# Kernel tuning notes

Measured on AMD Instinct MI355X. Metric: run time of the kernel, lower is better.

Reference implementation:

```python
import jax, jax.numpy as jnp
import numpy as np

B, L, D = 4, 4096, 256


def setup_inputs() -> dict:
    key = jax.random.key(0)
    k_x, k_q, k_k, k_v, k_w, k_b = jax.random.split(key, 6)
    s = 1.0 / np.sqrt(D)
    return {
        "x": jax.random.normal(k_x, (B, L, D), dtype=jnp.float32),
        "Wq": jax.random.normal(k_q, (D, D), dtype=jnp.float32) * s,   # nn.Linear weight (out,in)
        "Wk": jax.random.normal(k_k, (D, D), dtype=jnp.float32) * s,
        "Wv": jax.random.normal(k_v, (D, D), dtype=jnp.float32) * s,
        "w_mlp": jax.random.normal(k_w, (D,), dtype=jnp.float32) * s,  # Linear(D,1) weight
        "b_mlp": jnp.zeros((), dtype=jnp.float32),                     # Linear(D,1) bias
    }


def reference(x, Wq, Wk, Wv, w_mlp, b_mlp):
    # Projections (nn.Linear: y = x @ W.T, no bias)
    Q = jnp.einsum("bld,ed->ble", x, Wq)
    K = jnp.einsum("bld,ed->ble", x, Wk)
    V = jnp.einsum("bld,ed->ble", x, Wv)
    # score[b,i,j] = relu((Q[b,i]-K[b,j]) @ w_mlp + b_mlp)
    # decomposed: (Q-K)@w = Q@w - K@w  (exact same math, no (B,L,L,D) tensor)
    q_s = Q @ w_mlp  # (B,L)
    k_s = K @ w_mlp  # (B,L)
    scores = jax.nn.relu(q_s[:, :, None] - k_s[:, None, :] + b_mlp)  # (B,L,L)
    attn = jax.nn.softmax(scores, axis=-1)  # softmax over key axis j
    # out[b,i,d] = sum_j attn[b,i,j] * V[b,j,d]
    out = jnp.einsum("bij,bjd->bid", attn, V)
    return out  # dropout p=0.0 is identity
```

## Files before the change

### kernel.cpp

```cpp
#include <hip/hip_runtime.h>
#include <math.h>

#define BB 4
#define LL 4096
#define DD 256
#define NROWS (BB*LL)
#define CHUNK 32
#define NC (LL/CHUNK)
#define NB 8192

typedef __bf16 bf16x8 __attribute__((ext_vector_type(8)));
typedef __bf16 bf16x4 __attribute__((ext_vector_type(4)));
typedef float floatx4 __attribute__((ext_vector_type(4)));

__global__ void k_prep(const float* __restrict__ Wq, const float* __restrict__ Wk,
                       const float* __restrict__ Wv, const float* __restrict__ w,
                       float* __restrict__ u_part,
                       __bf16* __restrict__ Wh, __bf16* __restrict__ Wl) {
    __shared__ float wl[16];
    int d = threadIdx.x;
    int e0 = blockIdx.x * 16;
    if (d < 16) wl[d] = w[e0 + d];
    __syncthreads();
    float aq = 0.f, ak = 0.f;
    #pragma unroll
    for (int j = 0; j < 16; ++j) {
        float we = wl[j];
        aq = fmaf(Wq[(size_t)(e0 + j)*DD + d], we, aq);
        ak = fmaf(Wk[(size_t)(e0 + j)*DD + d], we, ak);
        float wv = Wv[(size_t)(e0 + j)*DD + d];
        __bf16 h = (__bf16)wv;
        Wh[(size_t)(e0 + j)*DD + d] = h;
        Wl[(size_t)(e0 + j)*DD + d] = (__bf16)(wv - (float)h);
    }
    u_part[(size_t)blockIdx.x*512 + d]       = aq;
    u_part[(size_t)blockIdx.x*512 + DD + d]  = ak;
}

__global__ void __launch_bounds__(256) k_gemm_mfma(
        const float* __restrict__ x,
        const __bf16* __restrict__ Wh, const __bf16* __restrict__ Wl,
        const float* __restrict__ u_part, const float* __restrict__ bmlp,
        float* __restrict__ V, float* __restrict__ a, float* __restrict__ c) {
    __shared__ __bf16 Ah[2][32*40];
    __shared__ __bf16 Al[2][32*40];
    __shared__ float4 ul[128];
    __shared__ float pros[512];
    const int tid = threadIdx.x;
    const int wave = tid >> 6, lane = tid & 63;
    const int rowBase = blockIdx.x * 32;
    const int colBase = blockIdx.y * 128;
    const int quad = lane >> 4, l16 = lane & 15;
    const int srow = tid >> 3, skq = (tid & 7) * 4;
    const bool doproj = (blockIdx.y == 0);

    if (doproj && tid < 128) {
        float4 s = make_float4(0.f, 0.f, 0.f, 0.f);
        #pragma unroll
        for (int g = 0; g < 16; ++g) {
            float4 p = *(const float4*)(u_part + (size_t)g*512 + tid*4);
            s.x += p.x; s.y += p.y; s.z += p.z; s.w += p.w;
        }
        ul[tid] = s;
    }
    __syncthreads();

    floatx4 acc[2][2];
    #pragma unroll
    for (int rt = 0; rt < 2; ++rt)
        #pragma unroll
        for (int ct = 0; ct < 2; ++ct)
            acc[rt][ct] = (floatx4){0.f, 0.f, 0.f, 0.f};
    float aq = 0.f, ak = 0.f;

    const float* xrow = x + (size_t)(rowBase + srow)*DD + skq;

    {
        float4 xv = *(const float4*)xrow;
        __bf16 h0 = (__bf16)xv.x, h1 = (__bf16)xv.y, h2 = (__bf16)xv.z, h3 = (__bf16)xv.w;
        bf16x4 hv = {h0, h1, h2, h3};
        bf16x4 lv = {(__bf16)(xv.x - (float)h0), (__bf16)(xv.y - (float)h1),
                     (__bf16)(xv.z - (float)h2), (__bf16)(xv.w - (float)h3)};
        *(bf16x4*)&Ah[0][srow*40 + skq] = hv;
        *(bf16x4*)&Al[0][srow*40 + skq] = lv;
        if (doproj) {
            float4 q4 = ul[(tid & 7)];
            float4 k4 = ul[64 + (tid & 7)];
            aq = fmaf(xv.x, q4.x, fmaf(xv.y, q4.y, fmaf(xv.z, q4.z, fmaf(xv.w, q4.w, aq))));
            ak = fmaf(xv.x, k4.x, fmaf(xv.y, k4.y, fmaf(xv.z, k4.z, fmaf(xv.w, k4.w, ak))));
        }
    }
    __syncthreads();

    for (int t = 0; t < 8; ++t) {
        const int k0 = t * 32;
        const int cur = t & 1;
        float4 xv;
        if (t < 7) xv = *(const float4*)(xrow + k0 + 32);
        bf16x8 ah[2], al[2];
        #pragma unroll
        for (int rt = 0; rt < 2; ++rt) {
            int m = rt*16 + l16;
            ah[rt] = *(bf16x8*)&Ah[cur][m*40 + quad*8];
            al[rt] = *(bf16x8*)&Al[cur][m*40 + quad*8];
        }
        if (t < 7) {
            __bf16 h0 = (__bf16)xv.x, h1 = (__bf16)xv.y, h2 = (__bf16)xv.z, h3 = (__bf16)xv.w;
            bf16x4 hv = {h0, h1, h2, h3};
            bf16x4 lv = {(__bf16)(xv.x - (float)h0), (__bf16)(xv.y - (float)h1),
                         (__bf16)(xv.z - (float)h2), (__bf16)(xv.w - (float)h3)};
            *(bf16x4*)&Ah[cur^1][srow*40 + skq] = hv;
            *(bf16x4*)&Al[cur^1][srow*40 + skq] = lv;
            if (doproj) {
                float4 q4 = ul[((k0 + 32) >> 2) + (tid & 7)];
                float4 k4 = ul[64 + ((k0 + 32) >> 2) + (tid & 7)];
                aq = fmaf(xv.x, q4.x, fmaf(xv.y, q4.y, fmaf(xv.z, q4.z, fmaf(xv.w, q4.w, aq))));
                ak = fmaf(xv.x, k4.x, fmaf(xv.y, k4.y, fmaf(xv.z, k4.z, fmaf(xv.w, k4.w, ak))));
            }
        }
        __syncthreads();
        #pragma unroll
        for (int ct = 0; ct < 2; ++ct) {
            int n = colBase + wave*32 + ct*16 + l16;
            bf16x8 bh = *(const bf16x8*)(Wh + (size_t)n*DD + k0 + quad*8);
            bf16x8 bl = *(const bf16x8*)(Wl + (size_t)n*DD + k0 + quad*8);
            #pragma unroll
            for (int rt = 0; rt < 2; ++rt) {
                acc[rt][ct] = __builtin_amdgcn_mfma_f32_16x16x32_bf16(ah[rt], bh, acc[rt][ct], 0, 0, 0);
                acc[rt][ct] = __builtin_amdgcn_mfma_f32_16x16x32_bf16(ah[rt], bl, acc[rt][ct], 0, 0, 0);
                acc[rt][ct] = __builtin_amdgcn_mfma_f32_16x16x32_bf16(al[rt], bh, acc[rt][ct], 0, 0, 0);
            }
        }
    }
    #pragma unroll
    for (int rt = 0; rt < 2; ++rt)
        #pragma unroll
        for (int ct = 0; ct < 2; ++ct)
            #pragma unroll
            for (int i = 0; i < 4; ++i) {
                int row = rowBase + rt*16 + quad*4 + i;
                int col = colBase + wave*32 + ct*16 + l16;
                V[(size_t)row*DD + col] = acc[rt][ct][i];
            }
    if (doproj) {
        __syncthreads();
        pros[tid] = aq;
        pros[256 + tid] = ak;
        __syncthreads();
        if (tid < 32) {
            float sa = 0.f, sc = 0.f;
            #pragma unroll
            for (int j = 0; j < 8; ++j) {
                sa += pros[tid*8 + j];
                sc += pros[256 + tid*8 + j];
            }
            a[rowBase + tid] = sa + bmlp[0];
            c[rowBase + tid] = sc;
        }
    }
}

__global__ void __launch_bounds__(1024) k_sortish(const float* __restrict__ c,
        int* __restrict__ binstart_g, int* __restrict__ perm,
        float* __restrict__ c_sorted, float* __restrict__ e_sorted,
        float* __restrict__ SE, float* __restrict__ hdr) {
    __shared__ int   hist[NB];
    __shared__ float esl[LL];
    __shared__ float scrf[64];
    int b = blockIdx.x, tid = threadIdx.x;
    int wave = tid >> 6, lane = tid & 63;
    int* scri = (int*)scrf;

    float4 cv = ((const float4*)(c + (size_t)b*LL))[tid];
    float cw[4] = {cv.x, cv.y, cv.z, cv.w};
    float mn = fminf(fminf(cw[0],cw[1]), fminf(cw[2],cw[3]));
    float mx = fmaxf(fmaxf(cw[0],cw[1]), fmaxf(cw[2],cw[3]));
    #pragma unroll
    for (int off = 32; off > 0; off >>= 1) {
        mn = fminf(mn, __shfl_down(mn, off));
        mx = fmaxf(mx, __shfl_down(mx, off));
    }
    if (lane == 0) { scrf[wave] = mn; scrf[32 + wave] = mx; }
    __syncthreads();
    if (wave == 0) {
        float m = (lane < 16) ? scrf[lane]      :  3.4e38f;
        float M = (lane < 16) ? scrf[32 + lane] : -3.4e38f;
        #pragma unroll
        for (int off = 32; off > 0; off >>= 1) {
            m = fminf(m, __shfl_down(m, off));
            M = fmaxf(M, __shfl_down(M, off));
        }
        if (lane == 0) { scrf[0] = m; scrf[1] = M; }
    }
    __syncthreads();
    float cmin = scrf[0], cmax = scrf[1];
    float scale = (float)NB / fmaxf(cmax - cmin, 1e-20f);
    __syncthreads();

    ((int4*)hist)[tid] = make_int4(0,0,0,0);
    ((int4*)hist)[tid + 1024] = make_int4(0,0,0,0);
    __syncthreads();

    int bins[4];
    #pragma unroll
    for (int u = 0; u < 4; ++u) {
        int bi = (int)((cw[u] - cmin) * scale);
        bi = bi < 0 ? 0 : (bi > NB-1 ? NB-1 : bi);
        bins[u] = bi;
        atomicAdd(&hist[bi], 1);
    }
    __syncthreads();

    int loc[8]; int base = 0;
    #pragma unroll
    for (int j = 0; j < 8; ++j) { loc[j] = base; base += hist[tid*8 + j]; }
    int incl = base;
    #pragma unroll
    for (int off = 1; off < 64; off <<= 1) {
        int t = __shfl_up(incl, off);
        if (lane >= off) incl += t;
    }
    if (lane == 63) scri[wave] = incl;
    __syncthreads();
    if (wave == 0) {
        int v = (lane < 16) ? scri[lane] : 0;
        int s = v;
        #pragma unroll
        for (int off = 1; off < 16; off <<= 1) {
            int t = __shfl_up(s, off);
            if (lane >= off) s += t;
        }
        if (lane < 16) scri[lane] = s - v;
    }
    __syncthreads();
    int thread_excl = (incl - base) + scri[wave];
    __syncthreads();
    #pragma unroll
    for (int j = 0; j < 8; ++j) {
        int bs = thread_excl + loc[j];
        binstart_g[(size_t)b*(NB+2) + tid*8 + j] = bs;
        hist[tid*8 + j] = bs;
    }
    if (tid == 0) {
        binstart_g[(size_t)b*(NB+2) + NB]     = LL;
        binstart_g[(size_t)b*(NB+2) + NB + 1] = LL;
        hdr[b*2 + 0] = cmin;
        hdr[b*2 + 1] = scale;
    }
    __syncthreads();

    #pragma unroll
    for (int u = 0; u < 4; ++u) {
        int i = tid*4 + u;
        int r = atomicAdd(&hist[bins[u]], 1);
        float e = expf(cmin - cw[u]);
        perm[(size_t)b*LL + r] = i;
        c_sorted[(size_t)b*LL + r] = cw[u];
        e_sorted[(size_t)b*LL + r] = e;
        esl[r] = e;
    }
    __syncthreads();

    float le[4]; float s0 = 0.f;
    #pragma unroll
    for (int u = 0; u < 4; ++u) { le[u] = s0; s0 += esl[tid*4 + u]; }
    float fincl = s0;
    #pragma unroll
    for (int off = 1; off < 64; off <<= 1) {
        float t = __shfl_up(fincl, off);
        if (lane >= off) fincl += t;
    }
    if (lane == 63) scrf[wave] = fincl;
    __syncthreads();
    if (wave == 0) {
        float v = (lane < 16) ? scrf[lane] : 0.f;
        float s = v;
        #pragma unroll
        for (int off = 1; off < 16; off <<= 1) {
            float t = __shfl_up(s, off);
            if (lane >= off) s += t;
        }
        if (lane < 16) scrf[lane] = s - v;
    }
    __syncthreads();
    float texcl = (fincl - s0) + scrf[wave];
    #pragma unroll
    for (int u = 0; u < 4; ++u)
        SE[(size_t)b*(LL+1) + tid*4 + u] = texcl + le[u];
    if (tid == 1023) SE[(size_t)b*(LL+1) + LL] = texcl + s0;
}

__global__ void k_scan(const float* __restrict__ V, const int* __restrict__ perm,
        const float* __restrict__ e_sorted,
        float* __restrict__ Pl, float* __restrict__ Pel,
        float* __restrict__ Tp, float* __restrict__ Te) {
    int b = blockIdx.y, q = blockIdx.x;
    int d = threadIdx.x;
    __shared__ int pj[CHUNK];
    __shared__ float pe[CHUNK];
    if (d < CHUNK) {
        pj[d] = perm[(size_t)b*LL + q*CHUNK + d];
        pe[d] = e_sorted[(size_t)b*LL + q*CHUNK + d];
    }
    __syncthreads();
    float vr[CHUNK];
    #pragma unroll
    for (int r = 0; r < CHUNK; ++r)
        vr[r] = V[((size_t)b*LL + pj[r]) * DD + d];
    float acc = 0.f, acce = 0.f;
    size_t kb = (size_t)b*LL + (size_t)q*CHUNK;
    #pragma unroll
    for (int r = 0; r < CHUNK; ++r) {
        size_t o = (kb + r) * DD + d;
        Pl[o]  = acc;
        Pel[o] = acce;
        acc += vr[r];
        acce = fmaf(pe[r], vr[r], acce);
    }
    size_t to = ((size_t)b*NC + q) * DD + d;
    Tp[to] = acc;
    Te[to] = acce;
}

__global__ void k_base(const float* __restrict__ Tp, const float* __restrict__ Te,
        float* __restrict__ baseP, float* __restrict__ basePe) {
    int q = blockIdx.x, b = blockIdx.y, d = threadIdx.x;
    float acc = 0.f, acce = 0.f;
    #pragma unroll 8
    for (int i = 0; i < q; ++i) {
        size_t ti = ((size_t)b*NC + i) * DD + d;
        acc += Tp[ti]; acce += Te[ti];
    }
    size_t o = ((size_t)b*(NC+1) + q) * DD + d;
    baseP[o] = acc; basePe[o] = acce;
}

__global__ void k_out(const float* __restrict__ a, const float* __restrict__ hdr,
                      const int* __restrict__ binstart,
                      const float* __restrict__ c_sorted, const float* __restrict__ e_sorted,
                      const int* __restrict__ perm, const float* __restrict__ V,
                      const float* __restrict__ SE,
                      const float* __restrict__ Pl, const float* __restrict__ Pel,
                      const float* __restrict__ baseP, const float* __restrict__ basePe,
                      float* __restrict__ out) {
    int row = blockIdx.x * 4 + (threadIdx.x >> 6);
    int lane = threadIdx.x & 63;
    int b = row >> 12;
    float ai = a[row];
    float cmin = hdr[b*2 + 0], scale = hdr[b*2 + 1];
    float t = (ai - cmin) * scale;
    int ib = t < 0.f ? 0 : (t >= (float)NB ? NB : (int)t);
    int k    = binstart[(size_t)b*(NB+2) + ib];
    int kend = binstart[(size_t)b*(NB+2) + ib + 1];
    float alpha = expf(cmin - ai);
    float Z = fmaf(alpha, (float)(LL - k), SE[(size_t)b*(LL+1) + k]);
    size_t db = (size_t)lane * 4;
    size_t totoff = ((size_t)b * (NC+1) + NC) * DD + db;
    float4 ptot  = *(const float4*)(baseP  + totoff);
    float4 pk, pek;
    if (k < LL) {
        int q = k >> 5;
        size_t po = ((size_t)b * LL + k) * DD + db;
        size_t bo = ((size_t)b * (NC+1) + q) * DD + db;
        float4 pl = *(const float4*)(Pl    + po);
        float4 bp = *(const float4*)(baseP + bo);
        float4 pe = *(const float4*)(Pel    + po);
        float4 be = *(const float4*)(basePe + bo);
        pk.x = pl.x + bp.x; pk.y = pl.y + bp.y; pk.z = pl.z + bp.z; pk.w = pl.w + bp.w;
        pek.x = pe.x + be.x; pek.y = pe.y + be.y; pek.z = pe.z + be.z; pek.w = pe.w + be.w;
    } else {
        pk = ptot;
        pek = *(const float4*)(basePe + totoff);
    }
    float4 num;
    num.x = fmaf(alpha, ptot.x - pk.x, pek.x);
    num.y = fmaf(alpha, ptot.y - pk.y, pek.y);
    num.z = fmaf(alpha, ptot.z - pk.z, pek.z);
    num.w = fmaf(alpha, ptot.w - pk.w, pek.w);
    for (int r = k; r < kend; ++r) {
        float cr = c_sorted[(size_t)b*LL + r];
        if (cr < ai) {
            float w = e_sorted[(size_t)b*LL + r] - alpha;
            int j = perm[(size_t)b*LL + r];
            float4 v = *(const float4*)(V + ((size_t)b*LL + j) * DD + db);
            num.x = fmaf(w, v.x, num.x);
            num.y = fmaf(w, v.y, num.y);
            num.z = fmaf(w, v.z, num.z);
            num.w = fmaf(w, v.w, num.w);
            Z += w;
        }
    }
    float invZ = 1.f / Z;
    float4 o;
    o.x = num.x * invZ; o.y = num.y * invZ; o.z = num.z * invZ; o.w = num.w * invZ;
    *(float4*)(out + (size_t)row * DD + db) = o;
}

extern "C" void kernel_launch(void* const* d_in, const int* in_sizes, int n_in,
                              void* d_out, int out_size, void* d_ws, size_t ws_size,
                              hipStream_t stream) {
    const float* x  = (const float*)d_in[0];
    const float* Wq = (const float*)d_in[1];
    const float* Wk = (const float*)d_in[2];
    const float* Wv = (const float*)d_in[3];
    const float* wm = (const float*)d_in[4];
    const float* bm = (const float*)d_in[5];
    float* out = (float*)d_out;
    float* ws = (float*)d_ws;

    size_t off = 0;
    auto alloc = [&](size_t n) {
        float* p = ws + off;
        off += (n + 255) & ~(size_t)255;
        return p;
    };
    float* u_part   = alloc(16*512);
    float* a        = alloc(NROWS);
    float* c        = alloc(NROWS);
    float* c_sorted = alloc(NROWS);
    float* e_sorted = alloc(NROWS);
    float* SE       = alloc((size_t)BB*(LL+1));
    int*   perm     = (int*)alloc(NROWS);
    int*   binstart = (int*)alloc((size_t)BB*(NB+2));
    float* hdr      = alloc(2*BB);
    float* V        = alloc((size_t)NROWS*DD);
    float* Pl       = alloc((size_t)NROWS*DD);
    float* Pel      = alloc((size_t)NROWS*DD);
    float* Tp       = alloc((size_t)BB*NC*DD);
    float* Te       = alloc((size_t)BB*NC*DD);
    float* baseP    = alloc((size_t)BB*(NC+1)*DD);
    float* basePe   = alloc((size_t)BB*(NC+1)*DD);
    __bf16* Wh      = (__bf16*)alloc((size_t)DD*DD/2);
    __bf16* Wl      = (__bf16*)alloc((size_t)DD*DD/2);

    hipLaunchKernelGGL(k_prep, dim3(16), dim3(DD), 0, stream, Wq, Wk, Wv, wm, u_part, Wh, Wl);
    hipLaunchKernelGGL(k_gemm_mfma, dim3(NROWS/32, 2), dim3(256), 0, stream,
                       x, Wh, Wl, u_part, bm, V, a, c);
    hipLaunchKernelGGL(k_sortish, dim3(BB), dim3(1024), 0, stream,
                       c, binstart, perm, c_sorted, e_sorted, SE, hdr);
    hipLaunchKernelGGL(k_scan, dim3(NC, BB), dim3(DD), 0, stream, V, perm, e_sorted, Pl, Pel, Tp, Te);
    hipLaunchKernelGGL(k_base, dim3(NC+1, BB), dim3(DD), 0, stream, Tp, Te, baseP, basePe);
    hipLaunchKernelGGL(k_out, dim3(NROWS/4), dim3(256), 0, stream,
                       a, hdr, binstart, c_sorted, e_sorted, perm, V,
                       SE, Pl, Pel, baseP, basePe, out);
}
```

Measured before the change: 135.1 us.

## Fuse chunk scan, base prefix and output into cooperative kernel with LDS prefixes

```diff
diff --git a/kernel.cpp b/kernel.cpp
--- a/kernel.cpp
+++ b/kernel.cpp
@@ -1,5 +1,8 @@
 #include <hip/hip_runtime.h>
+#include <hip/hip_cooperative_groups.h>
 #include <math.h>
+
+namespace cg = cooperative_groups;
 
 #define BB 4
 #define LL 4096
@@ -161,12 +164,16 @@
 }
 
 __global__ void __launch_bounds__(1024) k_sortish(const float* __restrict__ c,
-        int* __restrict__ binstart_g, int* __restrict__ perm,
+        const float* __restrict__ a,
+        int* __restrict__ perm,
         float* __restrict__ c_sorted, float* __restrict__ e_sorted,
-        float* __restrict__ SE, float* __restrict__ hdr) {
+        float* __restrict__ SE, float* __restrict__ hdr,
+        float4* __restrict__ rowrec, int* __restrict__ rbs_g) {
     __shared__ int   hist[NB];
     __shared__ float esl[LL];
     __shared__ float scrf[64];
+    __shared__ int   qhist[132];
+    __shared__ int   rbs[132];
     int b = blockIdx.x, tid = threadIdx.x;
     int wave = tid >> 6, lane = tid & 63;
     int* scri = (int*)scrf;
@@ -199,6 +206,7 @@
 
     ((int4*)hist)[tid] = make_int4(0,0,0,0);
     ((int4*)hist)[tid + 1024] = make_int4(0,0,0,0);
+    if (tid < 132) qhist[tid] = 0;
     __syncthreads();
 
     int bins[4];
@@ -238,14 +246,27 @@
     #pragma unroll
     for (int j = 0; j < 8; ++j) {
         int bs = thread_excl + loc[j];
-        binstart_g[(size_t)b*(NB+2) + tid*8 + j] = bs;
         hist[tid*8 + j] = bs;
     }
     if (tid == 0) {
-        binstart_g[(size_t)b*(NB+2) + NB]     = LL;
-        binstart_g[(size_t)b*(NB+2) + NB + 1] = LL;
         hdr[b*2 + 0] = cmin;
         hdr[b*2 + 1] = scale;
+    }
+    __syncthreads();
+
+    float4 av = ((const float4*)(a + (size_t)b*LL))[tid];
+    float aw[4] = {av.x, av.y, av.z, av.w};
+    int qq[4]; float4 rec[4];
+    #pragma unroll
+    for (int u = 0; u < 4; ++u) {
+        float t = (aw[u] - cmin) * scale;
+        int ibb = t < 0.f ? 0 : (t >= (float)NB ? NB : (int)t);
+        int k   = (ibb == NB)     ? LL : hist[ibb];
+        int ke  = (ibb >= NB - 1) ? LL : hist[ibb + 1];
+        qq[u] = k >> 5;
+        rec[u] = make_float4(aw[u], __int_as_float(k), __int_as_float(ke),
+                             __int_as_float(tid*4 + u));
+        atomicAdd(&qhist[qq[u]], 1);
     }
     __syncthreads();
 
@@ -261,6 +282,29 @@
     }
     __syncthreads();
 
+    if (wave == 0) {
+        int v0 = qhist[2*lane], v1 = qhist[2*lane+1];
+        int ps = v0 + v1;
+        int qi = ps;
+        #pragma unroll
+        for (int off = 1; off < 64; off <<= 1) {
+            int tu = __shfl_up(qi, off);
+            if (lane >= off) qi += tu;
+        }
+        rbs[2*lane]     = qi - ps;
+        rbs[2*lane + 1] = qi - v1;
+        if (lane == 63) { rbs[128] = qi; rbs[129] = qi + qhist[128]; }
+    }
+    __syncthreads();
+    if (tid < 129) qhist[tid] = rbs[tid];
+    if (tid < 130) rbs_g[b*130 + tid] = rbs[tid];
+    __syncthreads();
+    #pragma unroll
+    for (int u = 0; u < 4; ++u) {
+        int r = atomicAdd(&qhist[qq[u]], 1);
+        rowrec[(size_t)b*LL + r] = rec[u];
+    }
+
     float le[4]; float s0 = 0.f;
     #pragma unroll
     for (int u = 0; u < 4; ++u) { le[u] = s0; s0 += esl[tid*4 + u]; }
@@ -290,36 +334,147 @@
     if (tid == 1023) SE[(size_t)b*(LL+1) + LL] = texcl + s0;
 }
 
-__global__ void k_scan(const float* __restrict__ V, const int* __restrict__ perm,
-        const float* __restrict__ e_sorted,
-        float* __restrict__ Pl, float* __restrict__ Pel,
-        float* __restrict__ Tp, float* __restrict__ Te) {
-    int b = blockIdx.y, q = blockIdx.x;
-    int d = threadIdx.x;
-    __shared__ int pj[CHUNK];
-    __shared__ float pe[CHUNK];
-    if (d < CHUNK) {
-        pj[d] = perm[(size_t)b*LL + q*CHUNK + d];
-        pe[d] = e_sorted[(size_t)b*LL + q*CHUNK + d];
+__device__ __forceinline__ void chunk_out_phase(
+    int b, int q, int tid, const float (&vr)[CHUNK], const float* ev_l,
+    float* Plds, float* Pelds,
+    float* bp_l, float* be_l, float* pt_l, float* pe_l,
+    const float* __restrict__ baseP, const float* __restrict__ basePe,
+    const float4* __restrict__ rowrec, const int* __restrict__ rbs_g,
+    const float* __restrict__ SE, const float* __restrict__ hdr,
+    const float* __restrict__ c_sorted, const float* __restrict__ e_sorted,
+    const int* __restrict__ perm, const float* __restrict__ V,
+    float* __restrict__ out)
+{
+    {
+        size_t o  = ((size_t)b*(NC+1) + q)*DD + tid;
+        size_t ot = ((size_t)b*(NC+1) + NC)*DD + tid;
+        bp_l[tid] = baseP[o];  be_l[tid] = basePe[o];
+        pt_l[tid] = baseP[ot]; pe_l[tid] = basePe[ot];
+    }
+    float accp = 0.f, acce = 0.f;
+    #pragma unroll
+    for (int r = 0; r < CHUNK; ++r) {
+        Plds[r*DD + tid] = accp; Pelds[r*DD + tid] = acce;
+        accp += vr[r]; acce = fmaf(ev_l[r], vr[r], acce);
+    }
+    Plds[CHUNK*DD + tid] = accp; Pelds[CHUNK*DD + tid] = acce;
+    __syncthreads();
+    const int wave = tid >> 6, lane = tid & 63;
+    const int db = lane * 4;
+    const float cmin = hdr[b*2];
+    const float4 bp4 = *(const float4*)&bp_l[db];
+    const float4 be4 = *(const float4*)&be_l[db];
+    const float4 pt4 = *(const float4*)&pt_l[db];
+    const int rs = rbs_g[b*130 + q];
+    const int re = rbs_g[b*130 + q + ((q == NC-1) ? 2 : 1)];
+    for (int t = rs + wave; t < re; t += 4) {
+        float4 rr = rowrec[(size_t)b*LL + t];
+        float ai = rr.x;
+        int k    = __float_as_int(rr.y);
+        int kend = __float_as_int(rr.z);
+        int i    = __float_as_int(rr.w);
+        float alpha = expf(cmin - ai);
+        int local = k - q*CHUNK;
+        const float4 pl4 = *(const float4*)&Plds[local*DD + db];
+        const float4 pe4 = *(const float4*)&Pelds[local*DD + db];
+        float Z = fmaf(alpha, (float)(LL - k), SE[(size_t)b*(LL+1) + k]);
+        float4 num;
+        num.x = fmaf(alpha, pt4.x - (pl4.x + bp4.x), pe4.x + be4.x);
+        num.y = fmaf(alpha, pt4.y - (pl4.y + bp4.y), pe4.y + be4.y);
+        num.z = fmaf(alpha, pt4.z - (pl4.z + bp4.z), pe4.z + be4.z);
+        num.w = fmaf(alpha, pt4.w - (pl4.w + bp4.w), pe4.w + be4.w);
+        for (int r = k; r < kend; ++r) {
+            float cr = c_sorted[(size_t)b*LL + r];
+            if (cr < ai) {
+                float w = e_sorted[(size_t)b*LL + r] - alpha;
+                int j = perm[(size_t)b*LL + r];
+                float4 v = *(const float4*)(V + ((size_t)b*LL + j)*DD + db);
+                num.x = fmaf(w, v.x, num.x);
+                num.y = fmaf(w, v.y, num.y);
+                num.z = fmaf(w, v.z, num.z);
+                num.w = fmaf(w, v.w, num.w);
+                Z += w;
+            }
+        }
+        float invZ = 1.f / Z;
+        float4 o;
+        o.x = num.x * invZ; o.y = num.y * invZ; o.z = num.z * invZ; o.w = num.w * invZ;
+        *(float4*)(out + ((size_t)b*LL + i)*DD + db) = o;
+    }
+}
+
+__global__ void __launch_bounds__(256, 2) k_fused(
+    const float* __restrict__ V, const int* __restrict__ perm,
+    const float* __restrict__ e_sorted, const float* __restrict__ c_sorted,
+    const float4* __restrict__ rowrec, const int* __restrict__ rbs_g,
+    const float* __restrict__ SE, const float* __restrict__ hdr,
+    float* __restrict__ Tp, float* __restrict__ Te,
+    float* __restrict__ baseP, float* __restrict__ basePe,
+    float* __restrict__ out)
+{
+    __shared__ float Plds[(CHUNK+1)*DD];
+    __shared__ float Pelds[(CHUNK+1)*DD];
+    __shared__ float bp_l[DD], be_l[DD], pt_l[DD], pe_l[DD];
+    __shared__ float ev_l[CHUNK];
+    __shared__ int   pj_l[CHUNK];
+    const int q = blockIdx.x, b = blockIdx.y, tid = threadIdx.x;
+    if (tid < CHUNK) {
+        pj_l[tid] = perm[(size_t)b*LL + q*CHUNK + tid];
+        ev_l[tid] = e_sorted[(size_t)b*LL + q*CHUNK + tid];
     }
     __syncthreads();
     float vr[CHUNK];
     #pragma unroll
     for (int r = 0; r < CHUNK; ++r)
-        vr[r] = V[((size_t)b*LL + pj[r]) * DD + d];
-    float acc = 0.f, acce = 0.f;
-    size_t kb = (size_t)b*LL + (size_t)q*CHUNK;
+        vr[r] = V[((size_t)b*LL + pj_l[r])*DD + tid];
+    float sp = 0.f, se = 0.f;
+    #pragma unroll
+    for (int r = 0; r < CHUNK; ++r) { sp += vr[r]; se = fmaf(ev_l[r], vr[r], se); }
+    Tp[((size_t)b*NC + q)*DD + tid] = sp;
+    Te[((size_t)b*NC + q)*DD + tid] = se;
+    __threadfence();
+    cg::grid_group grid = cg::this_grid();
+    grid.sync();
+    if (q == 0) {
+        float ap = 0.f, ae = 0.f;
+        #pragma unroll 8
+        for (int i = 0; i < NC; ++i) {
+            size_t o  = ((size_t)b*(NC+1) + i)*DD + tid;
+            size_t ti = ((size_t)b*NC + i)*DD + tid;
+            baseP[o] = ap; basePe[o] = ae;
+            ap += Tp[ti]; ae += Te[ti];
+        }
+        baseP[((size_t)b*(NC+1) + NC)*DD + tid]  = ap;
+        basePe[((size_t)b*(NC+1) + NC)*DD + tid] = ae;
+    }
+    __threadfence();
+    grid.sync();
+    chunk_out_phase(b, q, tid, vr, ev_l, Plds, Pelds, bp_l, be_l, pt_l, pe_l,
+                    baseP, basePe, rowrec, rbs_g, SE, hdr,
+                    c_sorted, e_sorted, perm, V, out);
+}
+
+__global__ void __launch_bounds__(256) k_tot(
+    const float* __restrict__ V, const int* __restrict__ perm,
+    const float* __restrict__ e_sorted,
+    float* __restrict__ Tp, float* __restrict__ Te)
+{
+    __shared__ float ev_l[CHUNK];
+    __shared__ int   pj_l[CHUNK];
+    const int q = blockIdx.x, b = blockIdx.y, tid = threadIdx.x;
+    if (tid < CHUNK) {
+        pj_l[tid] = perm[(size_t)b*LL + q*CHUNK + tid];
+        ev_l[tid] = e_sorted[(size_t)b*LL + q*CHUNK + tid];
+    }
+    __syncthreads();
+    float sp = 0.f, se = 0.f;
     #pragma unroll
     for (int r = 0; r < CHUNK; ++r) {
-        size_t o = (kb + r) * DD + d;
-        Pl[o]  = acc;
-        Pel[o] = acce;
-        acc += vr[r];
-        acce = fmaf(pe[r], vr[r], acce);
-    }
-    size_t to = ((size_t)b*NC + q) * DD + d;
-    Tp[to] = acc;
-    Te[to] = acce;
+        float v = V[((size_t)b*LL + pj_l[r])*DD + tid];
+        sp += v; se = fmaf(ev_l[r], v, se);
+    }
+    Tp[((size_t)b*NC + q)*DD + tid] = sp;
+    Te[((size_t)b*NC + q)*DD + tid] = se;
 }
 
 __global__ void k_base(const float* __restrict__ Tp, const float* __restrict__ Te,
@@ -335,65 +490,32 @@
     baseP[o] = acc; basePe[o] = acce;
 }
 
-__global__ void k_out(const float* __restrict__ a, const float* __restrict__ hdr,
-                      const int* __restrict__ binstart,
-                      const float* __restrict__ c_sorted, const float* __restrict__ e_sorted,
-                      const int* __restrict__ perm, const float* __restrict__ V,
-                      const float* __restrict__ SE,
-                      const float* __restrict__ Pl, const float* __restrict__ Pel,
-                      const float* __restrict__ baseP, const float* __restrict__ basePe,
-                      float* __restrict__ out) {
-    int row = blockIdx.x * 4 + (threadIdx.x >> 6);
-    int lane = threadIdx.x & 63;
-    int b = row >> 12;
-    float ai = a[row];
-    float cmin = hdr[b*2 + 0], scale = hdr[b*2 + 1];
-    float t = (ai - cmin) * scale;
-    int ib = t < 0.f ? 0 : (t >= (float)NB ? NB : (int)t);
-    int k    = binstart[(size_t)b*(NB+2) + ib];
-    int kend = binstart[(size_t)b*(NB+2) + ib + 1];
-    float alpha = expf(cmin - ai);
-    float Z = fmaf(alpha, (float)(LL - k), SE[(size_t)b*(LL+1) + k]);
-    size_t db = (size_t)lane * 4;
-    size_t totoff = ((size_t)b * (NC+1) + NC) * DD + db;
-    float4 ptot  = *(const float4*)(baseP  + totoff);
-    float4 pk, pek;
-    if (k < LL) {
-        int q = k >> 5;
-        size_t po = ((size_t)b * LL + k) * DD + db;
-        size_t bo = ((size_t)b * (NC+1) + q) * DD + db;
-        float4 pl = *(const float4*)(Pl    + po);
-        float4 bp = *(const float4*)(baseP + bo);
-        float4 pe = *(const float4*)(Pel    + po);
-        float4 be = *(const float4*)(basePe + bo);
-        pk.x = pl.x + bp.x; pk.y = pl.y + bp.y; pk.z = pl.z + bp.z; pk.w = pl.w + bp.w;
-        pek.x = pe.x + be.x; pek.y = pe.y + be.y; pek.z = pe.z + be.z; pek.w = pe.w + be.w;
-    } else {
-        pk = ptot;
-        pek = *(const float4*)(basePe + totoff);
-    }
-    float4 num;
-    num.x = fmaf(alpha, ptot.x - pk.x, pek.x);
-    num.y = fmaf(alpha, ptot.y - pk.y, pek.y);
-    num.z = fmaf(alpha, ptot.z - pk.z, pek.z);
-    num.w = fmaf(alpha, ptot.w - pk.w, pek.w);
-    for (int r = k; r < kend; ++r) {
-        float cr = c_sorted[(size_t)b*LL + r];
-        if (cr < ai) {
-            float w = e_sorted[(size_t)b*LL + r] - alpha;
-            int j = perm[(size_t)b*LL + r];
-            float4 v = *(const float4*)(V + ((size_t)b*LL + j) * DD + db);
-            num.x = fmaf(w, v.x, num.x);
-            num.y = fmaf(w, v.y, num.y);
-            num.z = fmaf(w, v.z, num.z);
-            num.w = fmaf(w, v.w, num.w);
-            Z += w;
-        }
-    }
-    float invZ = 1.f / Z;
-    float4 o;
-    o.x = num.x * invZ; o.y = num.y * invZ; o.z = num.z * invZ; o.w = num.w * invZ;
-    *(float4*)(out + (size_t)row * DD + db) = o;
+__global__ void __launch_bounds__(256, 2) k_outf(
+    const float* __restrict__ V, const int* __restrict__ perm,
+    const float* __restrict__ e_sorted, const float* __restrict__ c_sorted,
+    const float4* __restrict__ rowrec, const int* __restrict__ rbs_g,
+    const float* __restrict__ SE, const float* __restrict__ hdr,
+    const float* __restrict__ baseP, const float* __restrict__ basePe,
+    float* __restrict__ out)
+{
+    __shared__ float Plds[(CHUNK+1)*DD];
+    __shared__ float Pelds[(CHUNK+1)*DD];
+    __shared__ float bp_l[DD], be_l[DD], pt_l[DD], pe_l[DD];
+    __shared__ float ev_l[CHUNK];
+    __shared__ int   pj_l[CHUNK];
+    const int q = blockIdx.x, b = blockIdx.y, tid = threadIdx.x;
+    if (tid < CHUNK) {
+        pj_l[tid] = perm[(size_t)b*LL + q*CHUNK + tid];
+        ev_l[tid] = e_sorted[(size_t)b*LL + q*CHUNK + tid];
+    }
+    __syncthreads();
+    float vr[CHUNK];
+    #pragma unroll
+    for (int r = 0; r < CHUNK; ++r)
+        vr[r] = V[((size_t)b*LL + pj_l[r])*DD + tid];
+    chunk_out_phase(b, q, tid, vr, ev_l, Plds, Pelds, bp_l, be_l, pt_l, pe_l,
+                    baseP, basePe, rowrec, rbs_g, SE, hdr,
+                    c_sorted, e_sorted, perm, V, out);
 }
 
 extern "C" void kernel_launch(void* const* d_in, const int* in_sizes, int n_in,
@@ -421,15 +543,14 @@
     float* e_sorted = alloc(NROWS);
     float* SE       = alloc((size_t)BB*(LL+1));
     int*   perm     = (int*)alloc(NROWS);
-    int*   binstart = (int*)alloc((size_t)BB*(NB+2));
     float* hdr      = alloc(2*BB);
     float* V        = alloc((size_t)NROWS*DD);
-    float* Pl       = alloc((size_t)NROWS*DD);
-    float* Pel      = alloc((size_t)NROWS*DD);
     float* Tp       = alloc((size_t)BB*NC*DD);
     float* Te       = alloc((size_t)BB*NC*DD);
     float* baseP    = alloc((size_t)BB*(NC+1)*DD);
     float* basePe   = alloc((size_t)BB*(NC+1)*DD);
+    float4* rowrec  = (float4*)alloc((size_t)NROWS*4);
+    int*   rbs_g    = (int*)alloc(BB*130);
     __bf16* Wh      = (__bf16*)alloc((size_t)DD*DD/2);
     __bf16* Wl      = (__bf16*)alloc((size_t)DD*DD/2);
 
@@ -437,10 +558,33 @@
     hipLaunchKernelGGL(k_gemm_mfma, dim3(NROWS/32, 2), dim3(256), 0, stream,
                        x, Wh, Wl, u_part, bm, V, a, c);
     hipLaunchKernelGGL(k_sortish, dim3(BB), dim3(1024), 0, stream,
-                       c, binstart, perm, c_sorted, e_sorted, SE, hdr);
-    hipLaunchKernelGGL(k_scan, dim3(NC, BB), dim3(DD), 0, stream, V, perm, e_sorted, Pl, Pel, Tp, Te);
-    hipLaunchKernelGGL(k_base, dim3(NC+1, BB), dim3(DD), 0, stream, Tp, Te, baseP, basePe);
-    hipLaunchKernelGGL(k_out, dim3(NROWS/4), dim3(256), 0, stream,
-                       a, hdr, binstart, c_sorted, e_sorted, perm, V,
-                       SE, Pl, Pel, baseP, basePe, out);
-}
+                       c, a, perm, c_sorted, e_sorted, SE, hdr, rowrec, rbs_g);
+
+    {
+        const float*  Vc    = V;
+        const int*    permc = perm;
+        const float*  ec    = e_sorted;
+        const float*  cc    = c_sorted;
+        const float4* rrc   = rowrec;
+        const int*    rbc   = rbs_g;
+        const float*  SEc   = SE;
+        const float*  hc    = hdr;
+        float* Tpp = Tp; float* Tee = Te; float* bP = baseP; float* bPe = basePe;
+        float* op = out;
+        void* kargs[] = { (void*)&Vc, (void*)&permc, (void*)&ec, (void*)&cc,
+                          (void*)&rrc, (void*)&rbc, (void*)&SEc, (void*)&hc,
+                          (void*)&Tpp, (void*)&Tee, (void*)&bP, (void*)&bPe,
+                          (void*)&op };
+        hipError_t cerr = hipLaunchCooperativeKernel((const void*)k_fused,
+                              dim3(NC, BB), dim3(DD), kargs, 0, stream);
+        if (cerr != hipSuccess) {
+            hipLaunchKernelGGL(k_tot, dim3(NC, BB), dim3(DD), 0, stream,
+                               V, perm, e_sorted, Tp, Te);
+            hipLaunchKernelGGL(k_base, dim3(NC+1, BB), dim3(DD), 0, stream,
+                               Tp, Te, baseP, basePe);
+            hipLaunchKernelGGL(k_outf, dim3(NC, BB), dim3(DD), 0, stream,
+                               V, perm, e_sorted, c_sorted, rowrec, rbs_g,
+                               SE, hdr, baseP, basePe, out);
+        }
+    }
+}
```

Result: slower. 316.5 us (+134.2%).

## Drop per-row prefix arrays; recompute in-chunk partial sums in output kernel

Applied to the files above, without the earlier changes.

```diff
diff --git a/kernel.cpp b/kernel.cpp
--- a/kernel.cpp
+++ b/kernel.cpp
@@ -5,21 +5,31 @@
 #define LL 4096
 #define DD 256
 #define NROWS (BB*LL)
-#define CHUNK 32
+#define CHUNK 16
 #define NC (LL/CHUNK)
-#define NB 8192
+#define NB 4096
 
 typedef __bf16 bf16x8 __attribute__((ext_vector_type(8)));
 typedef __bf16 bf16x4 __attribute__((ext_vector_type(4)));
 typedef float floatx4 __attribute__((ext_vector_type(4)));
 
+__device__ __forceinline__ unsigned encf(float f) {
+    unsigned u = __float_as_uint(f);
+    return (u & 0x80000000u) ? ~u : (u | 0x80000000u);
+}
+__device__ __forceinline__ float decf(unsigned u) {
+    return __uint_as_float((u & 0x80000000u) ? (u ^ 0x80000000u) : ~u);
+}
+
 __global__ void k_prep(const float* __restrict__ Wq, const float* __restrict__ Wk,
                        const float* __restrict__ Wv, const float* __restrict__ w,
                        float* __restrict__ u_part,
-                       __bf16* __restrict__ Wh, __bf16* __restrict__ Wl) {
+                       __bf16* __restrict__ Wh, __bf16* __restrict__ Wl,
+                       unsigned* __restrict__ hdru) {
     __shared__ float wl[16];
     int d = threadIdx.x;
     int e0 = blockIdx.x * 16;
+    if (blockIdx.x == 0 && d < 8) hdru[d] = (d & 1) ? 0u : 0xFFFFFFFFu;
     if (d < 16) wl[d] = w[e0 + d];
     __syncthreads();
     float aq = 0.f, ak = 0.f;
@@ -41,7 +51,8 @@
         const float* __restrict__ x,
         const __bf16* __restrict__ Wh, const __bf16* __restrict__ Wl,
         const float* __restrict__ u_part, const float* __restrict__ bmlp,
-        float* __restrict__ V, float* __restrict__ a, float* __restrict__ c) {
+        float* __restrict__ V, float* __restrict__ a, float* __restrict__ c,
+        unsigned* __restrict__ hdru) {
     __shared__ __bf16 Ah[2][32*40];
     __shared__ __bf16 Al[2][32*40];
     __shared__ float4 ul[128];
@@ -156,14 +167,26 @@
             }
             a[rowBase + tid] = sa + bmlp[0];
             c[rowBase + tid] = sc;
+            float mn = sc, mx = sc;
+            #pragma unroll
+            for (int off = 16; off > 0; off >>= 1) {
+                mn = fminf(mn, __shfl_down(mn, off));
+                mx = fmaxf(mx, __shfl_down(mx, off));
+            }
+            if (tid == 0) {
+                int bb = rowBase >> 12;
+                atomicMin(&hdru[bb*2 + 0], encf(mn));
+                atomicMax(&hdru[bb*2 + 1], encf(mx));
+            }
         }
     }
 }
 
 __global__ void __launch_bounds__(1024) k_sortish(const float* __restrict__ c,
+        const unsigned* __restrict__ hdru,
         int* __restrict__ binstart_g, int* __restrict__ perm,
         float* __restrict__ c_sorted, float* __restrict__ e_sorted,
-        float* __restrict__ SE, float* __restrict__ hdr) {
+        float* __restrict__ SE, float* __restrict__ hdrf) {
     __shared__ int   hist[NB];
     __shared__ float esl[LL];
     __shared__ float scrf[64];
@@ -173,32 +196,11 @@
 
     float4 cv = ((const float4*)(c + (size_t)b*LL))[tid];
     float cw[4] = {cv.x, cv.y, cv.z, cv.w};
-    float mn = fminf(fminf(cw[0],cw[1]), fminf(cw[2],cw[3]));
-    float mx = fmaxf(fmaxf(cw[0],cw[1]), fmaxf(cw[2],cw[3]));
-    #pragma unroll
-    for (int off = 32; off > 0; off >>= 1) {
-        mn = fminf(mn, __shfl_down(mn, off));
-        mx = fmaxf(mx, __shfl_down(mx, off));
-    }
-    if (lane == 0) { scrf[wave] = mn; scrf[32 + wave] = mx; }
-    __syncthreads();
-    if (wave == 0) {
-        float m = (lane < 16) ? scrf[lane]      :  3.4e38f;
-        float M = (lane < 16) ? scrf[32 + lane] : -3.4e38f;
-        #pragma unroll
-        for (int off = 32; off > 0; off >>= 1) {
-            m = fminf(m, __shfl_down(m, off));
-            M = fmaxf(M, __shfl_down(M, off));
-        }
-        if (lane == 0) { scrf[0] = m; scrf[1] = M; }
-    }
-    __syncthreads();
-    float cmin = scrf[0], cmax = scrf[1];
+    float cmin = decf(hdru[b*2 + 0]);
+    float cmax = decf(hdru[b*2 + 1]);
     float scale = (float)NB / fmaxf(cmax - cmin, 1e-20f);
-    __syncthreads();
 
     ((int4*)hist)[tid] = make_int4(0,0,0,0);
-    ((int4*)hist)[tid + 1024] = make_int4(0,0,0,0);
     __syncthreads();
 
     int bins[4];
@@ -211,9 +213,9 @@
     }
     __syncthreads();
 
-    int loc[8]; int base = 0;
-    #pragma unroll
-    for (int j = 0; j < 8; ++j) { loc[j] = base; base += hist[tid*8 + j]; }
+    int loc[4]; int base = 0;
+    #pragma unroll
+    for (int j = 0; j < 4; ++j) { loc[j] = base; base += hist[tid*4 + j]; }
     int incl = base;
     #pragma unroll
     for (int off = 1; off < 64; off <<= 1) {
@@ -236,16 +238,16 @@
     int thread_excl = (incl - base) + scri[wave];
     __syncthreads();
     #pragma unroll
-    for (int j = 0; j < 8; ++j) {
+    for (int j = 0; j < 4; ++j) {
         int bs = thread_excl + loc[j];
-        binstart_g[(size_t)b*(NB+2) + tid*8 + j] = bs;
-        hist[tid*8 + j] = bs;
+        binstart_g[(size_t)b*(NB+2) + tid*4 + j] = bs;
+        hist[tid*4 + j] = bs;
     }
     if (tid == 0) {
         binstart_g[(size_t)b*(NB+2) + NB]     = LL;
         binstart_g[(size_t)b*(NB+2) + NB + 1] = LL;
-        hdr[b*2 + 0] = cmin;
-        hdr[b*2 + 1] = scale;
+        hdrf[b*2 + 0] = cmin;
+        hdrf[b*2 + 1] = scale;
     }
     __syncthreads();
 
@@ -290,36 +292,27 @@
     if (tid == 1023) SE[(size_t)b*(LL+1) + LL] = texcl + s0;
 }
 
-__global__ void k_scan(const float* __restrict__ V, const int* __restrict__ perm,
-        const float* __restrict__ e_sorted,
-        float* __restrict__ Pl, float* __restrict__ Pel,
-        float* __restrict__ Tp, float* __restrict__ Te) {
-    int b = blockIdx.y, q = blockIdx.x;
-    int d = threadIdx.x;
-    __shared__ int pj[CHUNK];
-    __shared__ float pe[CHUNK];
-    if (d < CHUNK) {
-        pj[d] = perm[(size_t)b*LL + q*CHUNK + d];
-        pe[d] = e_sorted[(size_t)b*LL + q*CHUNK + d];
-    }
-    __syncthreads();
-    float vr[CHUNK];
-    #pragma unroll
-    for (int r = 0; r < CHUNK; ++r)
-        vr[r] = V[((size_t)b*LL + pj[r]) * DD + d];
-    float acc = 0.f, acce = 0.f;
-    size_t kb = (size_t)b*LL + (size_t)q*CHUNK;
+__global__ void __launch_bounds__(256) k_tot(
+    const float* __restrict__ V, const int* __restrict__ perm,
+    const float* __restrict__ e_sorted,
+    float* __restrict__ Tp, float* __restrict__ Te)
+{
+    __shared__ float ev_l[CHUNK];
+    __shared__ int   pj_l[CHUNK];
+    const int q = blockIdx.x, b = blockIdx.y, tid = threadIdx.x;
+    if (tid < CHUNK) {
+        pj_l[tid] = perm[(size_t)b*LL + q*CHUNK + tid];
+        ev_l[tid] = e_sorted[(size_t)b*LL + q*CHUNK + tid];
+    }
+    __syncthreads();
+    float sp = 0.f, se = 0.f;
     #pragma unroll
     for (int r = 0; r < CHUNK; ++r) {
-        size_t o = (kb + r) * DD + d;
-        Pl[o]  = acc;
-        Pel[o] = acce;
-        acc += vr[r];
-        acce = fmaf(pe[r], vr[r], acce);
-    }
-    size_t to = ((size_t)b*NC + q) * DD + d;
-    Tp[to] = acc;
-    Te[to] = acce;
+        float v = V[((size_t)b*LL + pj_l[r])*DD + tid];
+        sp += v; se = fmaf(ev_l[r], v, se);
+    }
+    Tp[((size_t)b*NC + q)*DD + tid] = sp;
+    Te[((size_t)b*NC + q)*DD + tid] = se;
 }
 
 __global__ void k_base(const float* __restrict__ Tp, const float* __restrict__ Te,
@@ -335,19 +328,18 @@
     baseP[o] = acc; basePe[o] = acce;
 }
 
-__global__ void k_out(const float* __restrict__ a, const float* __restrict__ hdr,
+__global__ void k_out(const float* __restrict__ a, const float* __restrict__ hdrf,
                       const int* __restrict__ binstart,
                       const float* __restrict__ c_sorted, const float* __restrict__ e_sorted,
                       const int* __restrict__ perm, const float* __restrict__ V,
                       const float* __restrict__ SE,
-                      const float* __restrict__ Pl, const float* __restrict__ Pel,
                       const float* __restrict__ baseP, const float* __restrict__ basePe,
                       float* __restrict__ out) {
     int row = blockIdx.x * 4 + (threadIdx.x >> 6);
     int lane = threadIdx.x & 63;
     int b = row >> 12;
     float ai = a[row];
-    float cmin = hdr[b*2 + 0], scale = hdr[b*2 + 1];
+    float cmin = hdrf[b*2 + 0], scale = hdrf[b*2 + 1];
     float t = (ai - cmin) * scale;
     int ib = t < 0.f ? 0 : (t >= (float)NB ? NB : (int)t);
     int k    = binstart[(size_t)b*(NB+2) + ib];
@@ -355,28 +347,29 @@
     float alpha = expf(cmin - ai);
     float Z = fmaf(alpha, (float)(LL - k), SE[(size_t)b*(LL+1) + k]);
     size_t db = (size_t)lane * 4;
-    size_t totoff = ((size_t)b * (NC+1) + NC) * DD + db;
-    float4 ptot  = *(const float4*)(baseP  + totoff);
-    float4 pk, pek;
-    if (k < LL) {
-        int q = k >> 5;
-        size_t po = ((size_t)b * LL + k) * DD + db;
-        size_t bo = ((size_t)b * (NC+1) + q) * DD + db;
-        float4 pl = *(const float4*)(Pl    + po);
-        float4 bp = *(const float4*)(baseP + bo);
-        float4 pe = *(const float4*)(Pel    + po);
-        float4 be = *(const float4*)(basePe + bo);
-        pk.x = pl.x + bp.x; pk.y = pl.y + bp.y; pk.z = pl.z + bp.z; pk.w = pl.w + bp.w;
-        pek.x = pe.x + be.x; pek.y = pe.y + be.y; pek.z = pe.z + be.z; pek.w = pe.w + be.w;
-    } else {
-        pk = ptot;
-        pek = *(const float4*)(basePe + totoff);
+    int q = k >> 4;
+    size_t bo = ((size_t)b*(NC+1) + q)*DD + db;
+    size_t to = ((size_t)b*(NC+1) + NC)*DD + db;
+    float4 bp = *(const float4*)(baseP  + bo);
+    float4 be = *(const float4*)(basePe + bo);
+    float4 pt = *(const float4*)(baseP  + to);
+    float4 pl = make_float4(0.f,0.f,0.f,0.f);
+    float4 pe = make_float4(0.f,0.f,0.f,0.f);
+    for (int r = (k & ~(CHUNK-1)); r < k; ++r) {
+        float e = e_sorted[(size_t)b*LL + r];
+        int j = perm[(size_t)b*LL + r];
+        float4 v = *(const float4*)(V + ((size_t)b*LL + j) * DD + db);
+        pl.x += v.x; pl.y += v.y; pl.z += v.z; pl.w += v.w;
+        pe.x = fmaf(e, v.x, pe.x);
+        pe.y = fmaf(e, v.y, pe.y);
+        pe.z = fmaf(e, v.z, pe.z);
+        pe.w = fmaf(e, v.w, pe.w);
     }
     float4 num;
-    num.x = fmaf(alpha, ptot.x - pk.x, pek.x);
-    num.y = fmaf(alpha, ptot.y - pk.y, pek.y);
-    num.z = fmaf(alpha, ptot.z - pk.z, pek.z);
-    num.w = fmaf(alpha, ptot.w - pk.w, pek.w);
+    num.x = fmaf(alpha, pt.x - (pl.x + bp.x), pe.x + be.x);
+    num.y = fmaf(alpha, pt.y - (pl.y + bp.y), pe.y + be.y);
+    num.z = fmaf(alpha, pt.z - (pl.z + bp.z), pe.z + be.z);
+    num.w = fmaf(alpha, pt.w - (pl.w + bp.w), pe.w + be.w);
     for (int r = k; r < kend; ++r) {
         float cr = c_sorted[(size_t)b*LL + r];
         if (cr < ai) {
@@ -422,10 +415,9 @@
     float* SE       = alloc((size_t)BB*(LL+1));
     int*   perm     = (int*)alloc(NROWS);
     int*   binstart = (int*)alloc((size_t)BB*(NB+2));
-    float* hdr      = alloc(2*BB);
+    float* hdrf     = alloc(2*BB);
+    unsigned* hdru  = (unsigned*)alloc(2*BB);
     float* V        = alloc((size_t)NROWS*DD);
-    float* Pl       = alloc((size_t)NROWS*DD);
-    float* Pel      = alloc((size_t)NROWS*DD);
     float* Tp       = alloc((size_t)BB*NC*DD);
     float* Te       = alloc((size_t)BB*NC*DD);
     float* baseP    = alloc((size_t)BB*(NC+1)*DD);
@@ -433,14 +425,17 @@
     __bf16* Wh      = (__bf16*)alloc((size_t)DD*DD/2);
     __bf16* Wl      = (__bf16*)alloc((size_t)DD*DD/2);
 
-    hipLaunchKernelGGL(k_prep, dim3(16), dim3(DD), 0, stream, Wq, Wk, Wv, wm, u_part, Wh, Wl);
+    hipLaunchKernelGGL(k_prep, dim3(16), dim3(DD), 0, stream,
+                       Wq, Wk, Wv, wm, u_part, Wh, Wl, hdru);
     hipLaunchKernelGGL(k_gemm_mfma, dim3(NROWS/32, 2), dim3(256), 0, stream,
-                       x, Wh, Wl, u_part, bm, V, a, c);
+                       x, Wh, Wl, u_part, bm, V, a, c, hdru);
     hipLaunchKernelGGL(k_sortish, dim3(BB), dim3(1024), 0, stream,
-                       c, binstart, perm, c_sorted, e_sorted, SE, hdr);
-    hipLaunchKernelGGL(k_scan, dim3(NC, BB), dim3(DD), 0, stream, V, perm, e_sorted, Pl, Pel, Tp, Te);
-    hipLaunchKernelGGL(k_base, dim3(NC+1, BB), dim3(DD), 0, stream, Tp, Te, baseP, basePe);
+                       c, hdru, binstart, perm, c_sorted, e_sorted, SE, hdrf);
+    hipLaunchKernelGGL(k_tot, dim3(NC, BB), dim3(256), 0, stream,
+                       V, perm, e_sorted, Tp, Te);
+    hipLaunchKernelGGL(k_base, dim3(NC+1, BB), dim3(256), 0, stream,
+                       Tp, Te, baseP, basePe);
     hipLaunchKernelGGL(k_out, dim3(NROWS/4), dim3(256), 0, stream,
-                       a, hdr, binstart, c_sorted, e_sorted, perm, V,
-                       SE, Pl, Pel, baseP, basePe, out);
-}
+                       a, hdrf, binstart, c_sorted, e_sorted, perm, V,
+                       SE, baseP, basePe, out);
+}
```

New measurement: 167.9 us. 1.24x slower.
